# Optimization experiments

Measured on AMD Instinct MI355X. Metric: run time of the kernel, lower is better.

Reference implementation:

```python
import jax, jax.numpy as jnp
import numpy as np

EPS = 1e-8


def setup_inputs() -> dict:
    key = jax.random.key(0)
    kx, kw, kb = jax.random.split(key, 3)
    B, S, K, N = 64, 4096, 256, 256
    x = jax.random.normal(kx, (B, S, K), dtype=jnp.float32)
    # Kaiming-uniform-ish init for weight (out_features, in_features)
    bound_w = np.sqrt(6.0 / K) / np.sqrt(1.0 + 5.0)  # kaiming_uniform with a=sqrt(5)
    weight = jax.random.uniform(kw, (N, K), dtype=jnp.float32, minval=-bound_w, maxval=bound_w)
    bound_b = 1.0 / np.sqrt(K)
    bias = jax.random.uniform(kb, (N,), dtype=jnp.float32, minval=-bound_b, maxval=bound_b)
    return {"x": x, "weight": weight, "bias": bias}


def reference(x, weight, bias):
    """LNS inference path of LNSLinear.

    log_out[m, n] = logsumexp_k(log(|x[m,k]|+eps) + log(|w[n,k]|+eps))
    out = sign(sign(x) @ sign(w).T) * exp(log_out) + bias
    Computed stably as log(exp(lx - mx) @ exp(lw - mw).T) + mx + mw.
    """
    orig_shape = x.shape
    K = weight.shape[1]
    xf = x.reshape(-1, K)                                  # [M, K]
    log_x = jnp.log(jnp.abs(xf) + EPS)                     # [M, K]
    x_sign = jnp.sign(xf)                                  # [M, K]
    log_w = jnp.log(jnp.abs(weight) + EPS)                 # [N, K]
    w_sign = jnp.sign(weight)                              # [N, K]

    mx = jnp.max(log_x, axis=-1, keepdims=True)            # [M, 1]
    mw = jnp.max(log_w, axis=-1, keepdims=True)            # [N, 1]
    # logsumexp over k without materializing [M, N, K]
    acc = jnp.einsum('mk,nk->mn', jnp.exp(log_x - mx), jnp.exp(log_w - mw))
    log_out = jnp.log(acc) + mx + mw.T                     # [M, N]

    out_sign = jnp.sign(jnp.einsum('mk,nk->mn', x_sign, w_sign))
    out = out_sign * jnp.exp(log_out) + bias
    return out.reshape(orig_shape[:-1] + (weight.shape[0],))
```

## Files before the change

### kernel.cpp

```cpp
#include <hip/hip_runtime.h>
#include <hip/hip_bf16.h>
#include <stdint.h>


#define K_DIM 256
#define N_DIM 256
#define BM 128
#define BN 128
#define BK 32
#define NKBLK 8

typedef float f32x4 __attribute__((ext_vector_type(4)));
typedef __bf16 bf16x8 __attribute__((ext_vector_type(8)));
typedef unsigned short u16x4v __attribute__((ext_vector_type(4)));
typedef unsigned short u16x8v __attribute__((ext_vector_type(8)));

__global__ void w_convert_kernel(const float* __restrict__ W, unsigned short* __restrict__ Wp) {
    int t = blockIdx.x * 256 + threadIdx.x;
    int n = t >> 6;
    int k = (t & 63) << 2;
    float4 v = *(const float4*)(W + (size_t)n * K_DIM + k);
    unsigned short* row = Wp + ((size_t)n * NKBLK + (k >> 5)) * 64;
    int pos = k & 31;
    float vv[4] = {v.x, v.y, v.z, v.w};
    u16x4v a, s;
#pragma unroll
    for (int j = 0; j < 4; ++j) {
        __bf16 h = (__bf16)__builtin_fabsf(vv[j]);
        a[j] = __builtin_bit_cast(unsigned short, h);
        unsigned int u = __float_as_uint(vv[j]);
        s[j] = (unsigned short)(0x3F80u | ((u >> 16) & 0x8000u));
    }
    *(u16x4v*)(row + pos) = a;
    *(u16x4v*)(row + 32 + pos) = s;
}

__device__ __forceinline__ void gload_lds16(const void* g, void* l) {
    __builtin_amdgcn_global_load_lds(
        (const __attribute__((address_space(1))) unsigned int*)g,
        (__attribute__((address_space(3))) unsigned int*)l, 16, 0, 0);
}

__global__ __launch_bounds__(256, 2)
void lns_gemm_kernel(const float* __restrict__ X, const unsigned short* __restrict__ Wp,
                     const float* __restrict__ bias, float* __restrict__ out) {
    __shared__ __attribute__((aligned(16))) float sA[2][BM * BK];
    __shared__ __attribute__((aligned(16))) unsigned short sB[2][BN * 64];

    const int tid  = threadIdx.x;
    const int lane = tid & 63;
    const int wave = tid >> 6;
    const int quad = lane >> 4;
    const int l16  = lane & 15;
    const int mb   = blockIdx.y;
    const int nb   = blockIdx.x;
    const int wm   = (wave >> 1) * 64;
    const int wn   = (wave & 1) * 64;

    const float* Ax = X + (size_t)(mb * BM) * K_DIM;
    const unsigned short* Bw = Wp + (size_t)(nb * BN) * (NKBLK * 64);

    const float* gA[4];
    const unsigned short* gB[4];
#pragma unroll
    for (int i = 0; i < 4; ++i) {
        int f = i * 256 + tid;
        int r = f >> 3;
        int g = (f & 7) ^ (r & 7);
        gA[i] = Ax + (size_t)r * K_DIM + g * 4;
        gB[i] = Bw + ((size_t)r * NKBLK) * 64 + g * 8;
    }

    f32x4 accP[4][4];
    f32x4 accS[4][4];
#pragma unroll
    for (int i = 0; i < 4; ++i)
#pragma unroll
        for (int j = 0; j < 4; ++j) {
            accP[i][j] = (f32x4)(0.0f);
            accS[i][j] = (f32x4)(0.0f);
        }

#pragma unroll
    for (int i = 0; i < 4; ++i) {
        gload_lds16(gA[i], &sA[0][(i * 256 + wave * 64) * 4]);
        gA[i] += BK;
    }
#pragma unroll
    for (int i = 0; i < 4; ++i) {
        gload_lds16(gB[i], &sB[0][(i * 256 + wave * 64) * 8]);
        gB[i] += 64;
    }

    for (int kb = 0; kb < NKBLK; ++kb) {
        const int cur = kb & 1;
        if (kb + 1 < NKBLK) {
            const int nxt = cur ^ 1;
#pragma unroll
            for (int i = 0; i < 4; ++i) {
                gload_lds16(gA[i], &sA[nxt][(i * 256 + wave * 64) * 4]);
                gA[i] += BK;
            }
#pragma unroll
            for (int i = 0; i < 4; ++i) {
                gload_lds16(gB[i], &sB[nxt][(i * 256 + wave * 64) * 8]);
                gB[i] += 64;
            }
            asm volatile("s_waitcnt vmcnt(8)\n\ts_barrier" ::: "memory");
        } else {
            asm volatile("s_waitcnt vmcnt(0)\n\ts_barrier" ::: "memory");
        }

        bf16x8 aab[4], asg[4], bab[4], bsg[4];
#pragma unroll
        for (int mi = 0; mi < 4; ++mi) {
            int m = wm + mi * 16 + l16;
            const float* rowp = &sA[cur][m * BK];
            int s0 = (2 * quad) ^ (m & 7);
            f32x4 f0 = *(const f32x4*)(rowp + s0 * 4);
            f32x4 f1 = *(const f32x4*)(rowp + (s0 ^ 1) * 4);
            u16x8v ab, sg;
#pragma unroll
            for (int j = 0; j < 4; ++j) {
                __bf16 h0 = (__bf16)__builtin_fabsf(f0[j]);
                __bf16 h1 = (__bf16)__builtin_fabsf(f1[j]);
                ab[j]     = __builtin_bit_cast(unsigned short, h0);
                ab[j + 4] = __builtin_bit_cast(unsigned short, h1);
                unsigned int u0 = __float_as_uint(f0[j]);
                unsigned int u1 = __float_as_uint(f1[j]);
                sg[j]     = (unsigned short)(0x3F80u | ((u0 >> 16) & 0x8000u));
                sg[j + 4] = (unsigned short)(0x3F80u | ((u1 >> 16) & 0x8000u));
            }
            aab[mi] = __builtin_bit_cast(bf16x8, ab);
            asg[mi] = __builtin_bit_cast(bf16x8, sg);
        }
#pragma unroll
        for (int ni = 0; ni < 4; ++ni) {
            int r = wn + ni * 16 + l16;
            const unsigned short* rp = &sB[cur][r * 64];
            int sa = quad ^ (r & 7);
            bab[ni] = __builtin_bit_cast(bf16x8, *(const u16x8v*)(rp + sa * 8));
            bsg[ni] = __builtin_bit_cast(bf16x8, *(const u16x8v*)(rp + (sa ^ 4) * 8));
        }
#pragma unroll
        for (int mi = 0; mi < 4; ++mi)
#pragma unroll
            for (int ni = 0; ni < 4; ++ni) {
                accP[mi][ni] = __builtin_amdgcn_mfma_f32_16x16x32_bf16(
                    aab[mi], bab[ni], accP[mi][ni], 0, 0, 0);
                accS[mi][ni] = __builtin_amdgcn_mfma_f32_16x16x32_bf16(
                    asg[mi], bsg[ni], accS[mi][ni], 0, 0, 0);
            }

        asm volatile("s_waitcnt lgkmcnt(0)\n\ts_barrier" ::: "memory");
    }

#pragma unroll
    for (int ni = 0; ni < 4; ++ni) {
        int n   = nb * BN + wn + ni * 16 + l16;
        float b = bias[n];
#pragma unroll
        for (int mi = 0; mi < 4; ++mi) {
            int mbase = mb * BM + wm + mi * 16 + quad * 4;
#pragma unroll
            for (int r = 0; r < 4; ++r) {
                float p = accP[mi][ni][r];
                float s = accS[mi][ni][r];
                float v = (s > 0.0f) ? p : ((s < 0.0f) ? -p : 0.0f);
                out[(size_t)(mbase + r) * N_DIM + n] = v + b;
            }
        }
    }
}

extern "C" void kernel_launch(void* const* d_in, const int* in_sizes, int n_in,
                              void* d_out, int out_size, void* d_ws, size_t ws_size,
                              hipStream_t stream) {
    const float* x    = (const float*)d_in[0];
    const float* w    = (const float*)d_in[1];
    const float* bias = (const float*)d_in[2];
    float* out        = (float*)d_out;
    unsigned short* Wp = (unsigned short*)d_ws;

    const int M = in_sizes[0] / K_DIM;

    w_convert_kernel<<<dim3(64, 1, 1), dim3(256, 1, 1), 0, stream>>>(w, Wp);

    dim3 grid(N_DIM / BN, M / BM, 1);
    dim3 block(256, 1, 1);
    lns_gemm_kernel<<<grid, block, 0, stream>>>(x, Wp, bias, out);
}
```

Baseline: 494.7 us.

## Load weights directly into registers and deepen the X LDS pipeline to four stages

The packed bf16 weight tile no longer goes through LDS. Each wave loads its B fragments straight from global memory into registers, one K-block ahead. The X tile now uses a four-stage LDS ring buffer filled by global_load_lds, which prefetches several K-blocks ahead and drops the per-iteration lgkmcnt wait. Sign packing for X uses a byte-permute instruction instead of per-element shifts and masks. This is meant to cut LDS traffic and synchronisation stalls, but it relies on implicit vmcnt ordering for LDS readiness and raises LDS usage to 64KB per block.

```diff
diff --git a/kernel.cpp b/kernel.cpp
--- a/kernel.cpp
+++ b/kernel.cpp
@@ -1,5 +1,4 @@
 #include <hip/hip_runtime.h>
-#include <hip/hip_bf16.h>
 #include <stdint.h>
 
 
@@ -14,6 +13,7 @@
 typedef __bf16 bf16x8 __attribute__((ext_vector_type(8)));
 typedef unsigned short u16x4v __attribute__((ext_vector_type(4)));
 typedef unsigned short u16x8v __attribute__((ext_vector_type(8)));
+typedef unsigned int u32x4v __attribute__((ext_vector_type(4)));
 
 __global__ void w_convert_kernel(const float* __restrict__ W, unsigned short* __restrict__ Wp) {
     int t = blockIdx.x * 256 + threadIdx.x;
@@ -41,11 +41,15 @@
         (__attribute__((address_space(3))) unsigned int*)l, 16, 0, 0);
 }
 
+__device__ __forceinline__ unsigned int sgnpk(float hi, float lo) {
+    return (__builtin_amdgcn_perm(__float_as_uint(hi), __float_as_uint(lo), 0x07000300u)
+            & 0x80008000u) | 0x3F803F80u;
+}
+
 __global__ __launch_bounds__(256, 2)
 void lns_gemm_kernel(const float* __restrict__ X, const unsigned short* __restrict__ Wp,
                      const float* __restrict__ bias, float* __restrict__ out) {
-    __shared__ __attribute__((aligned(16))) float sA[2][BM * BK];
-    __shared__ __attribute__((aligned(16))) unsigned short sB[2][BN * 64];
+    __shared__ __attribute__((aligned(16))) float sA[4][BM * BK];
 
     const int tid  = threadIdx.x;
     const int lane = tid & 63;
@@ -58,17 +62,23 @@
     const int wn   = (wave & 1) * 64;
 
     const float* Ax = X + (size_t)(mb * BM) * K_DIM;
-    const unsigned short* Bw = Wp + (size_t)(nb * BN) * (NKBLK * 64);
 
     const float* gA[4];
-    const unsigned short* gB[4];
+    int dstA[4];
 #pragma unroll
     for (int i = 0; i < 4; ++i) {
         int f = i * 256 + tid;
         int r = f >> 3;
         int g = (f & 7) ^ (r & 7);
         gA[i] = Ax + (size_t)r * K_DIM + g * 4;
-        gB[i] = Bw + ((size_t)r * NKBLK) * 64 + g * 8;
+        dstA[i] = (i * 256 + wave * 64) * 4;
+    }
+
+    const unsigned short* gB[4];
+#pragma unroll
+    for (int ni = 0; ni < 4; ++ni) {
+        int rw = nb * BN + wn + ni * 16 + l16;
+        gB[ni] = Wp + (size_t)rw * (NKBLK * 64) + quad * 8;
     }
 
     f32x4 accP[4][4];
@@ -81,37 +91,25 @@
             accS[i][j] = (f32x4)(0.0f);
         }
 
+    u16x8v bab[4], bsg[4];
 #pragma unroll
-    for (int i = 0; i < 4; ++i) {
-        gload_lds16(gA[i], &sA[0][(i * 256 + wave * 64) * 4]);
-        gA[i] += BK;
+    for (int ni = 0; ni < 4; ++ni) {
+        bab[ni] = *(const u16x8v*)(gB[ni]);
+        bsg[ni] = *(const u16x8v*)(gB[ni] + 32);
     }
+    asm volatile("" ::: "memory");
 #pragma unroll
-    for (int i = 0; i < 4; ++i) {
-        gload_lds16(gB[i], &sB[0][(i * 256 + wave * 64) * 8]);
-        gB[i] += 64;
-    }
+    for (int t = 0; t < 4; ++t)
+#pragma unroll
+        for (int i = 0; i < 4; ++i)
+            gload_lds16(gA[i] + t * BK, &sA[t][dstA[i]]);
+    asm volatile("s_waitcnt vmcnt(8)\n\ts_barrier" ::: "memory");
 
+#pragma unroll
     for (int kb = 0; kb < NKBLK; ++kb) {
-        const int cur = kb & 1;
-        if (kb + 1 < NKBLK) {
-            const int nxt = cur ^ 1;
-#pragma unroll
-            for (int i = 0; i < 4; ++i) {
-                gload_lds16(gA[i], &sA[nxt][(i * 256 + wave * 64) * 4]);
-                gA[i] += BK;
-            }
-#pragma unroll
-            for (int i = 0; i < 4; ++i) {
-                gload_lds16(gB[i], &sB[nxt][(i * 256 + wave * 64) * 8]);
-                gB[i] += 64;
-            }
-            asm volatile("s_waitcnt vmcnt(8)\n\ts_barrier" ::: "memory");
-        } else {
-            asm volatile("s_waitcnt vmcnt(0)\n\ts_barrier" ::: "memory");
-        }
+        const int cur = kb & 3;
 
-        bf16x8 aab[4], asg[4], bab[4], bsg[4];
+        bf16x8 aab[4], asg[4];
 #pragma unroll
         for (int mi = 0; mi < 4; ++mi) {
             int m = wm + mi * 16 + l16;
@@ -119,40 +117,44 @@
             int s0 = (2 * quad) ^ (m & 7);
             f32x4 f0 = *(const f32x4*)(rowp + s0 * 4);
             f32x4 f1 = *(const f32x4*)(rowp + (s0 ^ 1) * 4);
-            u16x8v ab, sg;
+            u16x8v ab;
 #pragma unroll
             for (int j = 0; j < 4; ++j) {
-                __bf16 h0 = (__bf16)__builtin_fabsf(f0[j]);
-                __bf16 h1 = (__bf16)__builtin_fabsf(f1[j]);
-                ab[j]     = __builtin_bit_cast(unsigned short, h0);
-                ab[j + 4] = __builtin_bit_cast(unsigned short, h1);
-                unsigned int u0 = __float_as_uint(f0[j]);
-                unsigned int u1 = __float_as_uint(f1[j]);
-                sg[j]     = (unsigned short)(0x3F80u | ((u0 >> 16) & 0x8000u));
-                sg[j + 4] = (unsigned short)(0x3F80u | ((u1 >> 16) & 0x8000u));
+                ab[j]     = __builtin_bit_cast(unsigned short, (__bf16)__builtin_fabsf(f0[j]));
+                ab[j + 4] = __builtin_bit_cast(unsigned short, (__bf16)__builtin_fabsf(f1[j]));
             }
             aab[mi] = __builtin_bit_cast(bf16x8, ab);
+            u32x4v sg;
+            sg[0] = sgnpk(f0[1], f0[0]);
+            sg[1] = sgnpk(f0[3], f0[2]);
+            sg[2] = sgnpk(f1[1], f1[0]);
+            sg[3] = sgnpk(f1[3], f1[2]);
             asg[mi] = __builtin_bit_cast(bf16x8, sg);
         }
-#pragma unroll
-        for (int ni = 0; ni < 4; ++ni) {
-            int r = wn + ni * 16 + l16;
-            const unsigned short* rp = &sB[cur][r * 64];
-            int sa = quad ^ (r & 7);
-            bab[ni] = __builtin_bit_cast(bf16x8, *(const u16x8v*)(rp + sa * 8));
-            bsg[ni] = __builtin_bit_cast(bf16x8, *(const u16x8v*)(rp + (sa ^ 4) * 8));
-        }
+
 #pragma unroll
         for (int mi = 0; mi < 4; ++mi)
 #pragma unroll
             for (int ni = 0; ni < 4; ++ni) {
                 accP[mi][ni] = __builtin_amdgcn_mfma_f32_16x16x32_bf16(
-                    aab[mi], bab[ni], accP[mi][ni], 0, 0, 0);
+                    aab[mi], __builtin_bit_cast(bf16x8, bab[ni]), accP[mi][ni], 0, 0, 0);
                 accS[mi][ni] = __builtin_amdgcn_mfma_f32_16x16x32_bf16(
-                    asg[mi], bsg[ni], accS[mi][ni], 0, 0, 0);
+                    asg[mi], __builtin_bit_cast(bf16x8, bsg[ni]), accS[mi][ni], 0, 0, 0);
             }
 
-        asm volatile("s_waitcnt lgkmcnt(0)\n\ts_barrier" ::: "memory");
+        if (kb + 1 < NKBLK) {
+#pragma unroll
+            for (int ni = 0; ni < 4; ++ni) {
+                bab[ni] = *(const u16x8v*)(gB[ni] + (kb + 1) * 64);
+                bsg[ni] = *(const u16x8v*)(gB[ni] + (kb + 1) * 64 + 32);
+            }
+            asm volatile("s_barrier" ::: "memory");
+            if (kb + 4 < NKBLK) {
+#pragma unroll
+                for (int i = 0; i < 4; ++i)
+                    gload_lds16(gA[i] + (kb + 4) * BK, &sA[(kb + 4) & 3][dstA[i]]);
+            }
+        }
     }
 
 #pragma unroll
```

Result: slower. 514.3 us (+4.0%).

## Convert X to bf16 once per tile into LDS via registers, halve BM

Applied to the files above, without the earlier changes.

X tiles now travel through registers: each thread loads floats, converts them to bf16 magnitude and sign planes once, and writes them into a padded LDS layout. Before, every wave converted its rows from fp32 in LDS on each read. BM drops to 64 and launch bounds rise to 4 blocks per CU, so more blocks are resident and LDS per block shrinks. The B tiles keep the async global-to-LDS path, with a reworked vmcnt and barrier schedule. The cost is that X loads are no longer async direct-to-LDS, and each B tile is reused across fewer M rows.

```diff
diff --git a/kernel.cpp b/kernel.cpp
--- a/kernel.cpp
+++ b/kernel.cpp
@@ -1,19 +1,20 @@
 #include <hip/hip_runtime.h>
-#include <hip/hip_bf16.h>
 #include <stdint.h>
 
 
 #define K_DIM 256
 #define N_DIM 256
-#define BM 128
+#define BM 64
 #define BN 128
 #define BK 32
 #define NKBLK 8
+#define AROW 72
 
 typedef float f32x4 __attribute__((ext_vector_type(4)));
 typedef __bf16 bf16x8 __attribute__((ext_vector_type(8)));
 typedef unsigned short u16x4v __attribute__((ext_vector_type(4)));
 typedef unsigned short u16x8v __attribute__((ext_vector_type(8)));
+typedef unsigned int u32x4v __attribute__((ext_vector_type(4)));
 
 __global__ void w_convert_kernel(const float* __restrict__ W, unsigned short* __restrict__ Wp) {
     int t = blockIdx.x * 256 + threadIdx.x;
@@ -41,10 +42,15 @@
         (__attribute__((address_space(3))) unsigned int*)l, 16, 0, 0);
 }
 
-__global__ __launch_bounds__(256, 2)
+__device__ __forceinline__ unsigned int sgnpk(float hi, float lo) {
+    return (__builtin_amdgcn_perm(__float_as_uint(hi), __float_as_uint(lo), 0x07000300u)
+            & 0x80008000u) | 0x3F803F80u;
+}
+
+__global__ __launch_bounds__(256, 4)
 void lns_gemm_kernel(const float* __restrict__ X, const unsigned short* __restrict__ Wp,
                      const float* __restrict__ bias, float* __restrict__ out) {
-    __shared__ __attribute__((aligned(16))) float sA[2][BM * BK];
+    __shared__ __attribute__((aligned(16))) unsigned short sA[2][BM * AROW];
     __shared__ __attribute__((aligned(16))) unsigned short sB[2][BN * 64];
 
     const int tid  = threadIdx.x;
@@ -54,105 +60,108 @@
     const int l16  = lane & 15;
     const int mb   = blockIdx.y;
     const int nb   = blockIdx.x;
-    const int wm   = (wave >> 1) * 64;
+    const int wm   = (wave >> 1) * 32;
     const int wn   = (wave & 1) * 64;
 
-    const float* Ax = X + (size_t)(mb * BM) * K_DIM;
-    const unsigned short* Bw = Wp + (size_t)(nb * BN) * (NKBLK * 64);
-
-    const float* gA[4];
+    const int ar = tid >> 2;
+    const int aq = tid & 3;
+    const float* gA = X + (size_t)(mb * BM + ar) * K_DIM + aq * 8;
+    unsigned short* const wA0 = &sA[0][ar * AROW + aq * 8];
+    unsigned short* const wA1 = &sA[1][ar * AROW + aq * 8];
+
     const unsigned short* gB[4];
+    int dstB[4];
 #pragma unroll
     for (int i = 0; i < 4; ++i) {
         int f = i * 256 + tid;
         int r = f >> 3;
         int g = (f & 7) ^ (r & 7);
-        gA[i] = Ax + (size_t)r * K_DIM + g * 4;
-        gB[i] = Bw + ((size_t)r * NKBLK) * 64 + g * 8;
-    }
-
-    f32x4 accP[4][4];
-    f32x4 accS[4][4];
-#pragma unroll
-    for (int i = 0; i < 4; ++i)
+        gB[i] = Wp + ((size_t)(nb * BN + r)) * (NKBLK * 64) + g * 8;
+        dstB[i] = (i * 256 + wave * 64) * 8;
+    }
+
+    f32x4 accP[2][4], accS[2][4];
+#pragma unroll
+    for (int i = 0; i < 2; ++i)
 #pragma unroll
         for (int j = 0; j < 4; ++j) {
             accP[i][j] = (f32x4)(0.0f);
             accS[i][j] = (f32x4)(0.0f);
         }
 
-#pragma unroll
-    for (int i = 0; i < 4; ++i) {
-        gload_lds16(gA[i], &sA[0][(i * 256 + wave * 64) * 4]);
-        gA[i] += BK;
-    }
-#pragma unroll
-    for (int i = 0; i < 4; ++i) {
-        gload_lds16(gB[i], &sB[0][(i * 256 + wave * 64) * 8]);
-        gB[i] += 64;
-    }
-
+    f32x4 ra[2];
+
+#define LOAD_A(kbv) do { \
+        const f32x4* _p = (const f32x4*)(gA + (kbv) * BK); \
+        ra[0] = _p[0]; ra[1] = _p[1]; \
+    } while (0)
+
+#define CONV_WRITE_A(dst) do { \
+        u16x8v _ab; \
+        _Pragma("unroll") \
+        for (int _j = 0; _j < 4; ++_j) { \
+            _ab[_j]     = __builtin_bit_cast(unsigned short, (__bf16)__builtin_fabsf(ra[0][_j])); \
+            _ab[_j + 4] = __builtin_bit_cast(unsigned short, (__bf16)__builtin_fabsf(ra[1][_j])); \
+        } \
+        u32x4v _sg; \
+        _sg[0] = sgnpk(ra[0][1], ra[0][0]); _sg[1] = sgnpk(ra[0][3], ra[0][2]); \
+        _sg[2] = sgnpk(ra[1][1], ra[1][0]); _sg[3] = sgnpk(ra[1][3], ra[1][2]); \
+        *(u16x8v*)(dst)        = _ab; \
+        *(u32x4v*)((dst) + 32) = _sg; \
+    } while (0)
+
+    LOAD_A(0);
+#pragma unroll
+    for (int i = 0; i < 4; ++i) gload_lds16(gB[i], &sB[0][dstB[i]]);
+    asm volatile("s_waitcnt vmcnt(4)" ::: "memory");
+    CONV_WRITE_A(wA0);
+    LOAD_A(1);
+#pragma unroll
+    for (int i = 0; i < 4; ++i) gload_lds16(gB[i] + 64, &sB[1][dstB[i]]);
+    asm volatile("s_waitcnt vmcnt(6) lgkmcnt(0)\n\ts_barrier" ::: "memory");
+
+#pragma unroll
     for (int kb = 0; kb < NKBLK; ++kb) {
         const int cur = kb & 1;
-        if (kb + 1 < NKBLK) {
-            const int nxt = cur ^ 1;
-#pragma unroll
-            for (int i = 0; i < 4; ++i) {
-                gload_lds16(gA[i], &sA[nxt][(i * 256 + wave * 64) * 4]);
-                gA[i] += BK;
-            }
-#pragma unroll
-            for (int i = 0; i < 4; ++i) {
-                gload_lds16(gB[i], &sB[nxt][(i * 256 + wave * 64) * 8]);
-                gB[i] += 64;
-            }
-            asm volatile("s_waitcnt vmcnt(8)\n\ts_barrier" ::: "memory");
-        } else {
-            asm volatile("s_waitcnt vmcnt(0)\n\ts_barrier" ::: "memory");
-        }
-
-        bf16x8 aab[4], asg[4], bab[4], bsg[4];
-#pragma unroll
-        for (int mi = 0; mi < 4; ++mi) {
-            int m = wm + mi * 16 + l16;
-            const float* rowp = &sA[cur][m * BK];
-            int s0 = (2 * quad) ^ (m & 7);
-            f32x4 f0 = *(const f32x4*)(rowp + s0 * 4);
-            f32x4 f1 = *(const f32x4*)(rowp + (s0 ^ 1) * 4);
-            u16x8v ab, sg;
-#pragma unroll
-            for (int j = 0; j < 4; ++j) {
-                __bf16 h0 = (__bf16)__builtin_fabsf(f0[j]);
-                __bf16 h1 = (__bf16)__builtin_fabsf(f1[j]);
-                ab[j]     = __builtin_bit_cast(unsigned short, h0);
-                ab[j + 4] = __builtin_bit_cast(unsigned short, h1);
-                unsigned int u0 = __float_as_uint(f0[j]);
-                unsigned int u1 = __float_as_uint(f1[j]);
-                sg[j]     = (unsigned short)(0x3F80u | ((u0 >> 16) & 0x8000u));
-                sg[j + 4] = (unsigned short)(0x3F80u | ((u1 >> 16) & 0x8000u));
-            }
-            aab[mi] = __builtin_bit_cast(bf16x8, ab);
-            asg[mi] = __builtin_bit_cast(bf16x8, sg);
+        const int nxt = cur ^ 1;
+
+        if (kb >= 1 && kb + 1 < NKBLK) {
+#pragma unroll
+            for (int i = 0; i < 4; ++i)
+                gload_lds16(gB[i] + (kb + 1) * 64, &sB[nxt][dstB[i]]);
+        }
+
+        bf16x8 aab[2], asg[2];
+#pragma unroll
+        for (int mi = 0; mi < 2; ++mi) {
+            const unsigned short* rp = &sA[cur][(wm + mi * 16 + l16) * AROW + quad * 8];
+            aab[mi] = __builtin_bit_cast(bf16x8, *(const u16x8v*)rp);
+            asg[mi] = __builtin_bit_cast(bf16x8, *(const u16x8v*)(rp + 32));
         }
 #pragma unroll
         for (int ni = 0; ni < 4; ++ni) {
             int r = wn + ni * 16 + l16;
             const unsigned short* rp = &sB[cur][r * 64];
             int sa = quad ^ (r & 7);
-            bab[ni] = __builtin_bit_cast(bf16x8, *(const u16x8v*)(rp + sa * 8));
-            bsg[ni] = __builtin_bit_cast(bf16x8, *(const u16x8v*)(rp + (sa ^ 4) * 8));
-        }
-#pragma unroll
-        for (int mi = 0; mi < 4; ++mi)
-#pragma unroll
-            for (int ni = 0; ni < 4; ++ni) {
-                accP[mi][ni] = __builtin_amdgcn_mfma_f32_16x16x32_bf16(
-                    aab[mi], bab[ni], accP[mi][ni], 0, 0, 0);
-                accS[mi][ni] = __builtin_amdgcn_mfma_f32_16x16x32_bf16(
-                    asg[mi], bsg[ni], accS[mi][ni], 0, 0, 0);
-            }
-
-        asm volatile("s_waitcnt lgkmcnt(0)\n\ts_barrier" ::: "memory");
+            bf16x8 bab = __builtin_bit_cast(bf16x8, *(const u16x8v*)(rp + sa * 8));
+            bf16x8 bsg = __builtin_bit_cast(bf16x8, *(const u16x8v*)(rp + (sa ^ 4) * 8));
+            accP[0][ni] = __builtin_amdgcn_mfma_f32_16x16x32_bf16(aab[0], bab, accP[0][ni], 0, 0, 0);
+            accP[1][ni] = __builtin_amdgcn_mfma_f32_16x16x32_bf16(aab[1], bab, accP[1][ni], 0, 0, 0);
+            accS[0][ni] = __builtin_amdgcn_mfma_f32_16x16x32_bf16(asg[0], bsg, accS[0][ni], 0, 0, 0);
+            accS[1][ni] = __builtin_amdgcn_mfma_f32_16x16x32_bf16(asg[1], bsg, accS[1][ni], 0, 0, 0);
+        }
+
+        if (kb + 1 < NKBLK) {
+            asm volatile("s_waitcnt vmcnt(4)" ::: "memory");
+            CONV_WRITE_A((kb & 1) ? wA0 : wA1);
+        }
+        if (kb + 2 < NKBLK) LOAD_A(kb + 2);
+        if (kb + 1 < NKBLK) {
+            if (kb + 2 < NKBLK)
+                asm volatile("s_waitcnt vmcnt(2) lgkmcnt(0)\n\ts_barrier" ::: "memory");
+            else
+                asm volatile("s_waitcnt vmcnt(0) lgkmcnt(0)\n\ts_barrier" ::: "memory");
+        }
     }
 
 #pragma unroll
@@ -160,7 +169,7 @@
         int n   = nb * BN + wn + ni * 16 + l16;
         float b = bias[n];
 #pragma unroll
-        for (int mi = 0; mi < 4; ++mi) {
+        for (int mi = 0; mi < 2; ++mi) {
             int mbase = mb * BM + wm + mi * 16 + quad * 4;
 #pragma unroll
             for (int r = 0; r < 4; ++r) {
```

After: 486.6 us. About the same (-1.6%).
